# Optimization experiments

Hardware: AMD Instinct MI355X
Metric: run time of the kernel (lower is better)

## Reference

```python
import jax, jax.numpy as jnp
import numpy as np

D = 1024
H = 16
EPS = 1e-5


def setup_inputs() -> dict:
    key = jax.random.key(0)
    ks = jax.random.split(key, 6)
    B, T, d = 4, 2048, D
    s = 0.02
    return {
        "x": jax.random.normal(ks[0], (B, T, d), jnp.float32),
        "w_attn": jax.random.normal(ks[1], (d, 3 * d), jnp.float32) * s,
        "w_o": jax.random.normal(ks[2], (d, d), jnp.float32) * s,
        "ln1_g": jnp.ones((d,), jnp.float32),
        "ln1_b": jnp.zeros((d,), jnp.float32),
        "ln2_g": jnp.ones((d,), jnp.float32),
        "ln2_b": jnp.zeros((d,), jnp.float32),
        "w_fc": jax.random.normal(ks[3], (d, 4 * d), jnp.float32) * s,
        "b_fc": jnp.zeros((4 * d,), jnp.float32),
        "w_proj": jax.random.normal(ks[4], (4 * d, d), jnp.float32) * s,
        "b_proj": jnp.zeros((d,), jnp.float32),
    }


def _layernorm(x, g, b):
    mu = jnp.mean(x, axis=-1, keepdims=True)
    var = jnp.mean(jnp.square(x - mu), axis=-1, keepdims=True)
    return (x - mu) * jax.lax.rsqrt(var + EPS) * g + b


def _attention(x, w_attn, w_o):
    B, T, d = x.shape
    hd = d // H
    qkv = x @ w_attn  # [B,T,3d]
    q, k, v = jnp.split(qkv, 3, axis=-1)
    q = q.reshape(B, T, H, hd).transpose(0, 2, 1, 3)  # [B,H,T,hd]
    k = k.reshape(B, T, H, hd).transpose(0, 2, 1, 3)
    v = v.reshape(B, T, H, hd).transpose(0, 2, 1, 3)
    att = jnp.einsum("bhqd,bhkd->bhqk", q, k) * (1.0 / np.sqrt(hd))
    mask = jnp.tril(jnp.ones((T, T), bool))
    att = jnp.where(mask, att, jnp.float32(-jnp.inf))
    att = jax.nn.softmax(att, axis=-1)
    y = jnp.einsum("bhqk,bhkd->bhqd", att, v)
    y = y.transpose(0, 2, 1, 3).reshape(B, T, d)
    return y @ w_o


def reference(x, w_attn, w_o, ln1_g, ln1_b, ln2_g, ln2_b, w_fc, b_fc, w_proj, b_proj):
    x = x + _attention(_layernorm(x, ln1_g, ln1_b), w_attn, w_o)
    h = _layernorm(x, ln2_g, ln2_b)
    h = jax.nn.gelu(h @ w_fc + b_fc, approximate=True)
    return x + h @ w_proj + b_proj
```

## Files before the change

kernel.cpp:

```cpp
#include <hip/hip_runtime.h>
#include <math.h>

#define D_MODEL 1024
#define NHEAD   16
#define HDIM    64
#define SEQ     2048
#define BATCH   4
#define NROWS   (BATCH*SEQ)

using bf16x8 = __attribute__((ext_vector_type(8))) short;
using bf16x4 = __attribute__((ext_vector_type(4))) short;
using f32x4  = __attribute__((ext_vector_type(4))) float;

__device__ __forceinline__ unsigned short f2bf(float f) {
    unsigned u = __float_as_uint(f);
    u += 0x7fffu + ((u >> 16) & 1u);
    return (unsigned short)(u >> 16);
}
__device__ __forceinline__ float bf2f(unsigned short h) {
    unsigned u = ((unsigned)h) << 16;
    return __uint_as_float(u);
}

#define ASYNC_COPY16(g, l) \
    __builtin_amdgcn_global_load_lds((__attribute__((address_space(1))) const void*)(g), \
                                     (__attribute__((address_space(3))) void*)(l), 16, 0, 0)

__global__ __launch_bounds__(256) void ln_kernel(const float* __restrict__ x,
                                                 const float* __restrict__ g,
                                                 const float* __restrict__ b,
                                                 unsigned short* __restrict__ out) {
    const int row = blockIdx.x;
    const int tid = threadIdx.x;
    const float4* x4 = (const float4*)(x + (size_t)row * D_MODEL);
    float4 v = x4[tid];
    float s  = v.x + v.y + v.z + v.w;
    float sq = v.x*v.x + v.y*v.y + v.z*v.z + v.w*v.w;
    #pragma unroll
    for (int off = 32; off >= 1; off >>= 1) {
        s  += __shfl_down(s,  off, 64);
        sq += __shfl_down(sq, off, 64);
    }
    __shared__ float rs[4], rq[4];
    const int wave = tid >> 6;
    if ((tid & 63) == 0) { rs[wave] = s; rq[wave] = sq; }
    __syncthreads();
    const float tot  = rs[0] + rs[1] + rs[2] + rs[3];
    const float totq = rq[0] + rq[1] + rq[2] + rq[3];
    const float mu   = tot * (1.0f / D_MODEL);
    const float var  = totq * (1.0f / D_MODEL) - mu * mu;
    const float rstd = rsqrtf(var + 1e-5f);
    const float4 gv = ((const float4*)g)[tid];
    const float4 bv = ((const float4*)b)[tid];
    unsigned short* o = out + (size_t)row * D_MODEL + tid * 4;
    o[0] = f2bf((v.x - mu) * rstd * gv.x + bv.x);
    o[1] = f2bf((v.y - mu) * rstd * gv.y + bv.y);
    o[2] = f2bf((v.z - mu) * rstd * gv.z + bv.z);
    o[3] = f2bf((v.w - mu) * rstd * gv.w + bv.w);
}

__global__ __launch_bounds__(256) void wt_kernel(const float* __restrict__ w,
                                                 unsigned short* __restrict__ wt,
                                                 int K, int N) {
    __shared__ float tile[32][33];
    const int n0 = blockIdx.x * 32, k0 = blockIdx.y * 32;
    const int tx = threadIdx.x & 31, ty = threadIdx.x >> 5;
    #pragma unroll
    for (int j = 0; j < 4; ++j)
        tile[ty + j * 8][tx] = w[(size_t)(k0 + ty + j * 8) * N + n0 + tx];
    __syncthreads();
    #pragma unroll
    for (int j = 0; j < 4; ++j)
        wt[(size_t)(n0 + ty + j * 8) * K + k0 + tx] = f2bf(tile[tx][ty + j * 8]);
}

__global__ __launch_bounds__(256) void gemm_qkv(const unsigned short* __restrict__ A,
                                                const unsigned short* __restrict__ Bt,
                                                unsigned short* __restrict__ qk_out,
                                                unsigned short* __restrict__ vt_out) {
    const int K = 1024;
    __shared__ __align__(16) unsigned short As[128 * 32];
    __shared__ __align__(16) unsigned short Bs[128 * 32];

    const int tid  = threadIdx.x;
    const int lane = tid & 63;
    const int wave = __builtin_amdgcn_readfirstlane(tid >> 6);
    const int quad = lane >> 4, l16 = lane & 15;
    const int wm = wave >> 1, wn = wave & 1;
    const int m0 = blockIdx.y * 128, n0 = blockIdx.x * 128;

    f32x4 acc[4][4] = {};

    const int rA = tid >> 2;
    const int p  = tid & 3;
    const int cs = (p ^ ((rA >> 1) & 3)) * 8;

    const unsigned short* Ag0 = A  + (size_t)(m0 + rA) * K + cs;
    const unsigned short* Ag1 = A  + (size_t)(m0 + rA + 64) * K + cs;
    const unsigned short* Bg0 = Bt + (size_t)(n0 + rA) * K + cs;
    const unsigned short* Bg1 = Bt + (size_t)(n0 + rA + 64) * K + cs;
    unsigned short* Al0 = As + tid * 8;
    unsigned short* Al1 = As + tid * 8 + 2048;
    unsigned short* Bl0 = Bs + tid * 8;
    unsigned short* Bl1 = Bs + tid * 8 + 2048;

    const int sw = (quad ^ ((l16 >> 1) & 3)) * 8;

    for (int kb = 0; kb < K; kb += 32) {
        ASYNC_COPY16(Ag0 + kb, Al0);
        ASYNC_COPY16(Ag1 + kb, Al1);
        ASYNC_COPY16(Bg0 + kb, Bl0);
        ASYNC_COPY16(Bg1 + kb, Bl1);
        __syncthreads();

        bf16x8 a[4], b[4];
        #pragma unroll
        for (int i = 0; i < 4; ++i)
            a[i] = *(const bf16x8*)&As[(wm * 64 + i * 16 + l16) * 32 + sw];
        #pragma unroll
        for (int j = 0; j < 4; ++j)
            b[j] = *(const bf16x8*)&Bs[(wn * 64 + j * 16 + l16) * 32 + sw];
        #pragma unroll
        for (int i = 0; i < 4; ++i)
            #pragma unroll
            for (int j = 0; j < 4; ++j)
                acc[i][j] = __builtin_amdgcn_mfma_f32_16x16x32_bf16(a[i], b[j], acc[i][j], 0, 0, 0);
        __syncthreads();
    }

    if (n0 < 2048) {
        const float sc = (n0 < 1024) ? 0.125f : 1.0f;
        #pragma unroll
        for (int i = 0; i < 4; ++i)
          #pragma unroll
          for (int j = 0; j < 4; ++j)
            #pragma unroll
            for (int r = 0; r < 4; ++r) {
                const int row = m0 + wm * 64 + i * 16 + quad * 4 + r;
                const int col = n0 + wn * 64 + j * 16 + l16;
                qk_out[(size_t)row * 2048 + col] = f2bf(acc[i][j][r] * sc);
            }
    } else {
        #pragma unroll
        for (int i = 0; i < 4; ++i)
          #pragma unroll
          for (int j = 0; j < 4; ++j) {
                const int dv  = n0 - 2048 + wn * 64 + j * 16 + l16;
                const int tok = m0 + wm * 64 + i * 16 + quad * 4;
                ushort4 pk;
                pk.x = f2bf(acc[i][j][0]); pk.y = f2bf(acc[i][j][1]);
                pk.z = f2bf(acc[i][j][2]); pk.w = f2bf(acc[i][j][3]);
                *(ushort4*)(vt_out + (size_t)dv * NROWS + tok) = pk;
            }
    }
}

template<bool GELU, bool OUT_BF16, bool PARTIAL>
__global__ __launch_bounds__(256) void gemm_bt(const unsigned short* __restrict__ A,
                                               const unsigned short* __restrict__ Bt,
                                               const float* __restrict__ bias,
                                               const float* __restrict__ resid,
                                               void* __restrict__ outp,
                                               int M, int N, int K, int Kslice) {
    __shared__ __align__(16) unsigned short As[128 * 32];
    __shared__ __align__(16) unsigned short Bs[128 * 32];

    const int tid  = threadIdx.x;
    const int lane = tid & 63;
    const int wave = __builtin_amdgcn_readfirstlane(tid >> 6);
    const int quad = lane >> 4, l16 = lane & 15;
    const int wm = wave >> 1, wn = wave & 1;
    const int m0 = blockIdx.y * 128, n0 = blockIdx.x * 128;
    const int kbeg = PARTIAL ? blockIdx.z * Kslice : 0;

    f32x4 acc[4][4] = {};

    const int rA = tid >> 2;
    const int p  = tid & 3;
    const int cs = (p ^ ((rA >> 1) & 3)) * 8;

    const unsigned short* Ag0 = A  + (size_t)(m0 + rA) * K + cs + kbeg;
    const unsigned short* Ag1 = A  + (size_t)(m0 + rA + 64) * K + cs + kbeg;
    const unsigned short* Bg0 = Bt + (size_t)(n0 + rA) * K + cs + kbeg;
    const unsigned short* Bg1 = Bt + (size_t)(n0 + rA + 64) * K + cs + kbeg;
    unsigned short* Al0 = As + tid * 8;
    unsigned short* Al1 = As + tid * 8 + 2048;
    unsigned short* Bl0 = Bs + tid * 8;
    unsigned short* Bl1 = Bs + tid * 8 + 2048;

    const int sw = (quad ^ ((l16 >> 1) & 3)) * 8;

    for (int kb = 0; kb < Kslice; kb += 32) {
        ASYNC_COPY16(Ag0 + kb, Al0);
        ASYNC_COPY16(Ag1 + kb, Al1);
        ASYNC_COPY16(Bg0 + kb, Bl0);
        ASYNC_COPY16(Bg1 + kb, Bl1);
        __syncthreads();

        bf16x8 a[4], b[4];
        #pragma unroll
        for (int i = 0; i < 4; ++i)
            a[i] = *(const bf16x8*)&As[(wm * 64 + i * 16 + l16) * 32 + sw];
        #pragma unroll
        for (int j = 0; j < 4; ++j)
            b[j] = *(const bf16x8*)&Bs[(wn * 64 + j * 16 + l16) * 32 + sw];
        #pragma unroll
        for (int i = 0; i < 4; ++i)
            #pragma unroll
            for (int j = 0; j < 4; ++j)
                acc[i][j] = __builtin_amdgcn_mfma_f32_16x16x32_bf16(a[i], b[j], acc[i][j], 0, 0, 0);
        __syncthreads();
    }

    unsigned short* outb = (unsigned short*)outp;
    if (PARTIAL) outb += (size_t)blockIdx.z * M * N;

    #pragma unroll
    for (int i = 0; i < 4; ++i)
      #pragma unroll
      for (int j = 0; j < 4; ++j)
        #pragma unroll
        for (int r = 0; r < 4; ++r) {
            const int row = m0 + wm * 64 + i * 16 + quad * 4 + r;
            const int col = n0 + wn * 64 + j * 16 + l16;
            float v = acc[i][j][r];
            if (PARTIAL) {
                outb[(size_t)row * N + col] = f2bf(v);
            } else {
                if (bias) v += bias[col];
                if (GELU) {
                    const float u = 0.7978845608028654f * (v + 0.044715f * v * v * v);
                    const float e = __expf(2.0f * u);
                    v = 0.5f * v * (2.0f - 2.0f / (e + 1.0f));
                }
                if (resid) v += resid[(size_t)row * N + col];
                if (OUT_BF16) outb[(size_t)row * N + col] = f2bf(v);
                else          ((float*)outp)[(size_t)row * N + col] = v;
            }
        }
}

__global__ __launch_bounds__(256, 2) void gemm_big(const unsigned short* __restrict__ A,
                                                   const unsigned short* __restrict__ Bt,
                                                   const float* __restrict__ bias,
                                                   unsigned short* __restrict__ outb,
                                                   int M, int N, int K) {
    __shared__ __align__(16) unsigned short As[256 * 32];
    __shared__ __align__(16) unsigned short Bs[128 * 32];

    const int tid  = threadIdx.x;
    const int lane = tid & 63;
    const int wave = __builtin_amdgcn_readfirstlane(tid >> 6);
    const int quad = lane >> 4, l16 = lane & 15;
    const int wm = wave >> 1, wn = wave & 1;
    const int m0 = blockIdx.y * 256, n0 = blockIdx.x * 128;

    f32x4 acc[8][4] = {};

    const int rr = tid >> 2;
    const int p  = tid & 3;
    const int cs = (p ^ ((rr >> 1) & 3)) * 8;

    const unsigned short* Ag[4];
    const unsigned short* Bg[2];
    #pragma unroll
    for (int i = 0; i < 4; ++i)
        Ag[i] = A + (size_t)(m0 + i * 64 + rr) * K + cs;
    #pragma unroll
    for (int i = 0; i < 2; ++i)
        Bg[i] = Bt + (size_t)(n0 + i * 64 + rr) * K + cs;

    const int sw = (quad ^ ((l16 >> 1) & 3)) * 8;

    for (int kb = 0; kb < K; kb += 32) {
        #pragma unroll
        for (int i = 0; i < 4; ++i)
            ASYNC_COPY16(Ag[i] + kb, As + i * 2048 + tid * 8);
        #pragma unroll
        for (int i = 0; i < 2; ++i)
            ASYNC_COPY16(Bg[i] + kb, Bs + i * 2048 + tid * 8);
        __syncthreads();

        bf16x8 b[4];
        #pragma unroll
        for (int j = 0; j < 4; ++j)
            b[j] = *(const bf16x8*)&Bs[(wn * 64 + j * 16 + l16) * 32 + sw];
        #pragma unroll
        for (int i = 0; i < 8; ++i) {
            bf16x8 a = *(const bf16x8*)&As[(wm * 128 + i * 16 + l16) * 32 + sw];
            #pragma unroll
            for (int j = 0; j < 4; ++j)
                acc[i][j] = __builtin_amdgcn_mfma_f32_16x16x32_bf16(a, b[j], acc[i][j], 0, 0, 0);
        }
        __syncthreads();
    }

    #pragma unroll
    for (int i = 0; i < 8; ++i)
      #pragma unroll
      for (int j = 0; j < 4; ++j)
        #pragma unroll
        for (int r = 0; r < 4; ++r) {
            const int row = m0 + wm * 128 + i * 16 + quad * 4 + r;
            const int col = n0 + wn * 64 + j * 16 + l16;
            float v = acc[i][j][r] + bias[col];
            const float u = 0.7978845608028654f * (v + 0.044715f * v * v * v);
            const float e = __expf(2.0f * u);
            v = 0.5f * v * (2.0f - 2.0f / (e + 1.0f));
            outb[(size_t)row * N + col] = f2bf(v);
        }
}

__global__ __launch_bounds__(256) void reduce_wo_ln2(const float* __restrict__ x,
                                                     const unsigned short* __restrict__ pw,
                                                     const float* __restrict__ g,
                                                     const float* __restrict__ bb,
                                                     float* __restrict__ out,
                                                     unsigned short* __restrict__ lnout) {
    const int row = blockIdx.x;
    const int tid = threadIdx.x;
    const size_t base = (size_t)row * D_MODEL + tid * 4;
    const size_t stride = (size_t)NROWS * D_MODEL;
    float4 v = *(const float4*)(x + base);
    #pragma unroll
    for (int z = 0; z < 4; ++z) {
        ushort4 a = *(const ushort4*)(pw + z * stride + base);
        v.x += bf2f(a.x); v.y += bf2f(a.y); v.z += bf2f(a.z); v.w += bf2f(a.w);
    }
    *(float4*)(out + base) = v;

    float s  = v.x + v.y + v.z + v.w;
    float sq = v.x*v.x + v.y*v.y + v.z*v.z + v.w*v.w;
    #pragma unroll
    for (int off = 32; off >= 1; off >>= 1) {
        s  += __shfl_down(s,  off, 64);
        sq += __shfl_down(sq, off, 64);
    }
    __shared__ float rs[4], rq[4];
    const int wave = tid >> 6;
    if ((tid & 63) == 0) { rs[wave] = s; rq[wave] = sq; }
    __syncthreads();
    const float tot  = rs[0] + rs[1] + rs[2] + rs[3];
    const float totq = rq[0] + rq[1] + rq[2] + rq[3];
    const float mu   = tot * (1.0f / D_MODEL);
    const float var  = totq * (1.0f / D_MODEL) - mu * mu;
    const float rstd = rsqrtf(var + 1e-5f);
    const float4 gv = ((const float4*)g)[tid];
    const float4 bv = ((const float4*)bb)[tid];
    unsigned short* o = lnout + (size_t)row * D_MODEL + tid * 4;
    o[0] = f2bf((v.x - mu) * rstd * gv.x + bv.x);
    o[1] = f2bf((v.y - mu) * rstd * gv.y + bv.y);
    o[2] = f2bf((v.z - mu) * rstd * gv.z + bv.z);
    o[3] = f2bf((v.w - mu) * rstd * gv.w + bv.w);
}

__global__ __launch_bounds__(256) void reduce_kernel(float* __restrict__ out,
                                                     const unsigned short* __restrict__ p0,
                                                     const unsigned short* __restrict__ p1,
                                                     const float* __restrict__ bias) {
    const int row = blockIdx.x;
    const int c0 = threadIdx.x * 4;
    const size_t base = (size_t)row * D_MODEL + c0;
    float4 o = *(float4*)(out + base);
    ushort4 a = *(const ushort4*)(p0 + base);
    ushort4 b = *(const ushort4*)(p1 + base);
    const float4 bs = *(const float4*)(bias + c0);
    o.x += bs.x + bf2f(a.x) + bf2f(b.x);
    o.y += bs.y + bf2f(a.y) + bf2f(b.y);
    o.z += bs.z + bf2f(a.z) + bf2f(b.z);
    o.w += bs.w + bf2f(a.w) + bf2f(b.w);
    *(float4*)(out + base) = o;
}

__global__ __launch_bounds__(256) void attn_kernel(const unsigned short* __restrict__ qk,
                                                   const unsigned short* __restrict__ VT,
                                                   unsigned short* __restrict__ y) {
    __shared__ __align__(16) unsigned short Qs[128 * 64];
    __shared__ __align__(16) unsigned short Ks[64 * 64];
    __shared__ __align__(16) unsigned short Vs[80 * 64];
    __shared__ __align__(16) unsigned short Ps[128 * 68];

    const int tid  = threadIdx.x;
    const int lane = tid & 63, w = tid >> 6;
    const int quad = lane >> 4, l16 = lane & 15;
    const int s7   = l16 & 7;
    const int pc0  = (quad ^ s7) * 8;
    const int pc1  = ((quad + 4) ^ s7) * 8;
    const int srow = tid >> 3, sp = tid & 7;

    const int pairidx = blockIdx.x;
    const int bh = blockIdx.y;
    const int b = bh >> 4, h = bh & 15;
    const size_t rowbase = (size_t)b * SEQ;
    const unsigned short* Qbase = qk + h * 64;
    const unsigned short* Kbase = qk + 1024 + h * 64;
    const unsigned short* Vbase = VT + (size_t)(h * 64) * NROWS + b * SEQ;

    #pragma unroll
    for (int e = 0; e < 4; ++e) {
        const int off = tid * 4 + e;
        Vs[4096 + off] = (off < 64) ? (unsigned short)0x3F80 : (unsigned short)0;
    }

    for (int phase = 0; phase < 2; ++phase) {
        const int Q = phase ? pairidx : (15 - pairidx);
        const int nkt = 2 * Q + 2;
        const int qg0 = Q * 128;

        #pragma unroll
        for (int i = 0; i < 4; ++i) {
            const int row = i * 32 + srow;
            const int c = sp ^ (row & 7);
            ASYNC_COPY16(Qbase + (rowbase + qg0 + row) * 2048 + c * 8,
                         (char*)Qs + i * 4096 + tid * 16);
        }
        __syncthreads();

        bf16x8 aq[2][2];
        #pragma unroll
        for (int sub = 0; sub < 2; ++sub) {
            const int qrow = sub * 64 + w * 16 + l16;
            aq[sub][0] = *(const bf16x8*)&Qs[qrow * 64 + pc0];
            aq[sub][1] = *(const bf16x8*)&Qs[qrow * 64 + pc1];
        }

        f32x4 o[2][5] = {};

        for (int kt = 0; kt < nkt; ++kt) {
            #pragma unroll
            for (int i = 0; i < 2; ++i) {
                const int row = i * 32 + srow;
                const int c = sp ^ (row & 7);
                ASYNC_COPY16(Kbase + (rowbase + kt * 64 + row) * 2048 + c * 8,
                             (char*)Ks + i * 4096 + tid * 16);
                ASYNC_COPY16(Vbase + (size_t)row * NROWS + kt * 64 + c * 8,
                             (char*)Vs + i * 4096 + tid * 16);
            }
            __syncthreads();

            bf16x8 bk[4][2];
            #pragma unroll
            for (int cb = 0; cb < 4; ++cb) {
                const int krow = cb * 16 + l16;
                bk[cb][0] = *(const bf16x8*)&Ks[krow * 64 + pc0];
                bk[cb][1] = *(const bf16x8*)&Ks[krow * 64 + pc1];
            }

            #pragma unroll
            for (int sub = 0; sub < 2; ++sub) {
                if (kt > 2 * Q + sub) continue;
                f32x4 s[4] = {};
                #pragma unroll
                for (int cb = 0; cb < 4; ++cb) {
                    s[cb] = __builtin_amdgcn_mfma_f32_16x16x32_bf16(aq[sub][0], bk[cb][0], s[cb], 0, 0, 0);
                    s[cb] = __builtin_amdgcn_mfma_f32_16x16x32_bf16(aq[sub][1], bk[cb][1], s[cb], 0, 0, 0);
                }
                const int prow0 = sub * 64 + w * 16 + quad * 4;
                if (kt == 2 * Q + sub) {
                    const int qg = qg0 + prow0;
                    const int kg = kt * 64 + l16;
                    #pragma unroll
                    for (int cb = 0; cb < 4; ++cb)
                        #pragma unroll
                        for (int r = 0; r < 4; ++r) {
                            const float e = __expf(s[cb][r]);
                            const float pv = (kg + cb * 16 > qg + r) ? 0.0f : e;
                            Ps[(prow0 + r) * 68 + cb * 16 + l16] = f2bf(pv);
                        }
                } else {
                    #pragma unroll
                    for (int cb = 0; cb < 4; ++cb)
                        #pragma unroll
                        for (int r = 0; r < 4; ++r)
                            Ps[(prow0 + r) * 68 + cb * 16 + l16] = f2bf(__expf(s[cb][r]));
                }
            }
            __syncthreads();

            bf16x8 bv[5][2];
            #pragma unroll
            for (int db = 0; db < 5; ++db) {
                const int vrow = db * 16 + l16;
                bv[db][0] = *(const bf16x8*)&Vs[vrow * 64 + pc0];
                bv[db][1] = *(const bf16x8*)&Vs[vrow * 64 + pc1];
            }
            #pragma unroll
            for (int sub = 0; sub < 2; ++sub) {
                if (kt > 2 * Q + sub) continue;
                const unsigned short* pb = &Ps[(sub * 64 + w * 16 + l16) * 68];
                bf16x8 ap0, ap1;
                *(bf16x4*)&ap0       = *(const bf16x4*)(pb + quad * 8);
                *((bf16x4*)&ap0 + 1) = *(const bf16x4*)(pb + quad * 8 + 4);
                *(bf16x4*)&ap1       = *(const bf16x4*)(pb + 32 + quad * 8);
                *((bf16x4*)&ap1 + 1) = *(const bf16x4*)(pb + 32 + quad * 8 + 4);
                #pragma unroll
                for (int db = 0; db < 5; ++db) {
                    o[sub][db] = __builtin_amdgcn_mfma_f32_16x16x32_bf16(ap0, bv[db][0], o[sub][db], 0, 0, 0);
                    o[sub][db] = __builtin_amdgcn_mfma_f32_16x16x32_bf16(ap1, bv[db][1], o[sub][db], 0, 0, 0);
                }
            }
            __syncthreads();
        }

        #pragma unroll
        for (int sub = 0; sub < 2; ++sub)
            #pragma unroll
            for (int r = 0; r < 4; ++r) {
                const float lsum = __shfl(o[sub][4][r], lane & 48);
                const float rinv = 1.0f / lsum;
                const int trow = qg0 + sub * 64 + w * 16 + quad * 4 + r;
                unsigned short* yp = y + (rowbase + trow) * (size_t)D_MODEL + h * 64 + l16;
                #pragma unroll
                for (int db = 0; db < 4; ++db)
                    yp[db * 16] = f2bf(o[sub][db][r] * rinv);
            }
    }
}

extern "C" void kernel_launch(void* const* d_in, const int* in_sizes, int n_in,
                              void* d_out, int out_size, void* d_ws, size_t ws_size,
                              hipStream_t stream) {
    (void)in_sizes; (void)n_in; (void)out_size; (void)ws_size;
    const float* x      = (const float*)d_in[0];
    const float* w_attn = (const float*)d_in[1];
    const float* w_o    = (const float*)d_in[2];
    const float* ln1_g  = (const float*)d_in[3];
    const float* ln1_b  = (const float*)d_in[4];
    const float* ln2_g  = (const float*)d_in[5];
    const float* ln2_b  = (const float*)d_in[6];
    const float* w_fc   = (const float*)d_in[7];
    const float* b_fc   = (const float*)d_in[8];
    const float* w_proj = (const float*)d_in[9];
    const float* b_proj = (const float*)d_in[10];
    float* out = (float*)d_out;

    char* ws = (char*)d_ws;
    const size_t MiB = 1048576;
    unsigned short* ln_buf  = (unsigned short*)ws;
    unsigned short* qkbuf   = (unsigned short*)(ws + 16 * MiB);
    unsigned short* VTbuf   = (unsigned short*)(ws + 48 * MiB);
    unsigned short* wt_attn = (unsigned short*)(ws + 64 * MiB);
    unsigned short* hbuf    = (unsigned short*)(ws + 64 * MiB);
    unsigned short* wt_o    = (unsigned short*)(ws + 126 * MiB);
    unsigned short* pw      = (unsigned short*)(ws + 16 * MiB);
    unsigned short* wt_fc   = (unsigned short*)(ws + 16 * MiB);
    unsigned short* wt_proj = (unsigned short*)(ws + 24 * MiB);
    unsigned short* pp      = (unsigned short*)(ws + 32 * MiB);

    wt_kernel<<<dim3(3072 / 32, 1024 / 32), 256, 0, stream>>>(w_attn, wt_attn, 1024, 3072);
    wt_kernel<<<dim3(1024 / 32, 1024 / 32), 256, 0, stream>>>(w_o, wt_o, 1024, 1024);

    ln_kernel<<<NROWS, 256, 0, stream>>>(x, ln1_g, ln1_b, ln_buf);

    gemm_qkv<<<dim3(3072 / 128, NROWS / 128), 256, 0, stream>>>(
        ln_buf, wt_attn, qkbuf, VTbuf);

    attn_kernel<<<dim3(8, BATCH * NHEAD), 256, 0, stream>>>(qkbuf, VTbuf, ln_buf);

    gemm_bt<false, true, true><<<dim3(1024 / 128, NROWS / 128, 4), 256, 0, stream>>>(
        ln_buf, wt_o, nullptr, nullptr, pw, NROWS, 1024, 1024, 256);
    reduce_wo_ln2<<<NROWS, 256, 0, stream>>>(x, pw, ln2_g, ln2_b, out, ln_buf);

    wt_kernel<<<dim3(4096 / 32, 1024 / 32), 256, 0, stream>>>(w_fc, wt_fc, 1024, 4096);
    wt_kernel<<<dim3(1024 / 32, 4096 / 32), 256, 0, stream>>>(w_proj, wt_proj, 4096, 1024);

    gemm_big<<<dim3(4096 / 128, NROWS / 256), 256, 0, stream>>>(
        ln_buf, wt_fc, b_fc, hbuf, NROWS, 4096, 1024);

    gemm_bt<false, true, true><<<dim3(1024 / 128, NROWS / 128, 2), 256, 0, stream>>>(
        hbuf, wt_proj, nullptr, nullptr, pp, NROWS, 1024, 4096, 2048);
    reduce_kernel<<<NROWS, 256, 0, stream>>>(
        out, pp, pp + (size_t)NROWS * 1024, b_proj);
}
```

Before: 578.3 us.

## Swap GEMM grid axes to M-major and use 3-way split-K for proj

```diff
diff --git a/kernel.cpp b/kernel.cpp
--- a/kernel.cpp
+++ b/kernel.cpp
@@ -87,7 +87,7 @@
     const int wave = __builtin_amdgcn_readfirstlane(tid >> 6);
     const int quad = lane >> 4, l16 = lane & 15;
     const int wm = wave >> 1, wn = wave & 1;
-    const int m0 = blockIdx.y * 128, n0 = blockIdx.x * 128;
+    const int m0 = blockIdx.x * 128, n0 = blockIdx.y * 128;
 
     f32x4 acc[4][4] = {};
 
@@ -170,8 +170,10 @@
     const int wave = __builtin_amdgcn_readfirstlane(tid >> 6);
     const int quad = lane >> 4, l16 = lane & 15;
     const int wm = wave >> 1, wn = wave & 1;
-    const int m0 = blockIdx.y * 128, n0 = blockIdx.x * 128;
+    const int m0 = blockIdx.x * 128, n0 = blockIdx.y * 128;
     const int kbeg = PARTIAL ? blockIdx.z * Kslice : 0;
+    const int klen = PARTIAL ? ((blockIdx.z == gridDim.z - 1) ? (K - kbeg) : Kslice)
+                             : K;
 
     f32x4 acc[4][4] = {};
 
@@ -190,7 +192,7 @@
 
     const int sw = (quad ^ ((l16 >> 1) & 3)) * 8;
 
-    for (int kb = 0; kb < Kslice; kb += 32) {
+    for (int kb = 0; kb < klen; kb += 32) {
         ASYNC_COPY16(Ag0 + kb, Al0);
         ASYNC_COPY16(Ag1 + kb, Al1);
         ASYNC_COPY16(Bg0 + kb, Bl0);
@@ -253,7 +255,7 @@
     const int wave = __builtin_amdgcn_readfirstlane(tid >> 6);
     const int quad = lane >> 4, l16 = lane & 15;
     const int wm = wave >> 1, wn = wave & 1;
-    const int m0 = blockIdx.y * 256, n0 = blockIdx.x * 128;
+    const int m0 = blockIdx.x * 256, n0 = blockIdx.y * 128;
 
     f32x4 acc[8][4] = {};
 
@@ -355,20 +357,20 @@
 }
 
 __global__ __launch_bounds__(256) void reduce_kernel(float* __restrict__ out,
-                                                     const unsigned short* __restrict__ p0,
-                                                     const unsigned short* __restrict__ p1,
+                                                     const unsigned short* __restrict__ pp,
                                                      const float* __restrict__ bias) {
     const int row = blockIdx.x;
     const int c0 = threadIdx.x * 4;
     const size_t base = (size_t)row * D_MODEL + c0;
+    const size_t stride = (size_t)NROWS * D_MODEL;
     float4 o = *(float4*)(out + base);
-    ushort4 a = *(const ushort4*)(p0 + base);
-    ushort4 b = *(const ushort4*)(p1 + base);
     const float4 bs = *(const float4*)(bias + c0);
-    o.x += bs.x + bf2f(a.x) + bf2f(b.x);
-    o.y += bs.y + bf2f(a.y) + bf2f(b.y);
-    o.z += bs.z + bf2f(a.z) + bf2f(b.z);
-    o.w += bs.w + bf2f(a.w) + bf2f(b.w);
+    o.x += bs.x; o.y += bs.y; o.z += bs.z; o.w += bs.w;
+    #pragma unroll
+    for (int z = 0; z < 3; ++z) {
+        ushort4 a = *(const ushort4*)(pp + z * stride + base);
+        o.x += bf2f(a.x); o.y += bf2f(a.y); o.z += bf2f(a.z); o.w += bf2f(a.w);
+    }
     *(float4*)(out + base) = o;
 }
 
@@ -543,32 +545,31 @@
     unsigned short* hbuf    = (unsigned short*)(ws + 64 * MiB);
     unsigned short* wt_o    = (unsigned short*)(ws + 126 * MiB);
     unsigned short* pw      = (unsigned short*)(ws + 16 * MiB);
-    unsigned short* wt_fc   = (unsigned short*)(ws + 16 * MiB);
-    unsigned short* wt_proj = (unsigned short*)(ws + 24 * MiB);
-    unsigned short* pp      = (unsigned short*)(ws + 32 * MiB);
+    unsigned short* wt_fc   = (unsigned short*)(ws + 48 * MiB);
+    unsigned short* wt_proj = (unsigned short*)(ws + 56 * MiB);
+    unsigned short* pp      = (unsigned short*)ws;
 
     wt_kernel<<<dim3(3072 / 32, 1024 / 32), 256, 0, stream>>>(w_attn, wt_attn, 1024, 3072);
     wt_kernel<<<dim3(1024 / 32, 1024 / 32), 256, 0, stream>>>(w_o, wt_o, 1024, 1024);
 
     ln_kernel<<<NROWS, 256, 0, stream>>>(x, ln1_g, ln1_b, ln_buf);
 
-    gemm_qkv<<<dim3(3072 / 128, NROWS / 128), 256, 0, stream>>>(
+    gemm_qkv<<<dim3(NROWS / 128, 3072 / 128), 256, 0, stream>>>(
         ln_buf, wt_attn, qkbuf, VTbuf);
 
     attn_kernel<<<dim3(8, BATCH * NHEAD), 256, 0, stream>>>(qkbuf, VTbuf, ln_buf);
 
-    gemm_bt<false, true, true><<<dim3(1024 / 128, NROWS / 128, 4), 256, 0, stream>>>(
+    gemm_bt<false, true, true><<<dim3(NROWS / 128, 1024 / 128, 4), 256, 0, stream>>>(
         ln_buf, wt_o, nullptr, nullptr, pw, NROWS, 1024, 1024, 256);
     reduce_wo_ln2<<<NROWS, 256, 0, stream>>>(x, pw, ln2_g, ln2_b, out, ln_buf);
 
     wt_kernel<<<dim3(4096 / 32, 1024 / 32), 256, 0, stream>>>(w_fc, wt_fc, 1024, 4096);
     wt_kernel<<<dim3(1024 / 32, 4096 / 32), 256, 0, stream>>>(w_proj, wt_proj, 4096, 1024);
 
-    gemm_big<<<dim3(4096 / 128, NROWS / 256), 256, 0, stream>>>(
+    gemm_big<<<dim3(NROWS / 256, 4096 / 128), 256, 0, stream>>>(
         ln_buf, wt_fc, b_fc, hbuf, NROWS, 4096, 1024);
 
-    gemm_bt<false, true, true><<<dim3(1024 / 128, NROWS / 128, 2), 256, 0, stream>>>(
-        hbuf, wt_proj, nullptr, nullptr, pp, NROWS, 1024, 4096, 2048);
-    reduce_kernel<<<NROWS, 256, 0, stream>>>(
-        out, pp, pp + (size_t)NROWS * 1024, b_proj);
-}
+    gemm_bt<false, true, true><<<dim3(NROWS / 128, 1024 / 128, 3), 256, 0, stream>>>(
+        hbuf, wt_proj, nullptr, nullptr, pp, NROWS, 1024, 4096, 1344);
+    reduce_kernel<<<NROWS, 256, 0, stream>>>(out, pp, b_proj);
+}
```

Result: faster. 546.3 us (-5.5%).
